# Performance work log

Measured on AMD Instinct MI355X. Metric: run time of the kernel, lower is better.

## Reference

```python
import jax, jax.numpy as jnp
import numpy as np

N = 4096          # num_nodes
M = 131072        # num_edges (chain + random)
H = 64            # hidden_size of DerivConstrainedPerceptron
DMIN = 0.5
DMAX = 2.0
LO = 1.0 / DMAX   # min slope of h_inv
HI = 1.0 / DMIN   # max slope of h_inv
MITR = 30         # fixed iteration count (early-exit at eps in the original; 30 iters converge far below eps here)
RIDGE = 1e-6      # numerical ridge on grounded Laplacian


def _h_inv(y, logits, w_raw, b):
    # Derivative-constrained perceptron: h_inv'(y) = LO + (HI-LO)*sum_k p_k*sigmoid(w_k*y+b_k) in (LO, HI).
    p = jax.nn.softmax(logits)                     # (H,)
    w = jax.nn.softplus(w_raw) + 1e-3              # (H,) positive slopes
    s = jax.nn.softplus(y[..., None] * w + b)      # (m, d, H)
    return LO * y + (HI - LO) * jnp.einsum('mdh,h->md', s, p / w)


def _chol_grounded(src, dst, w, n):
    # Dense weighted graph Laplacian L = A diag(w) A^T built by scatter-add, grounded at the last node.
    L = jnp.zeros((n, n), w.dtype)
    L = L.at[src, src].add(w).at[dst, dst].add(w)
    L = L.at[src, dst].add(-w).at[dst, src].add(-w)
    Lg = L[:-1, :-1] + RIDGE * jnp.eye(n - 1, dtype=w.dtype)
    return jnp.linalg.cholesky(Lg)


def _solve_grounded(c, rhs):
    # Solve L phi = rhs with the grounded node's potential fixed to 0 (valid for balanced rhs; only
    # potential differences phi[src]-phi[dst] are used, which equal A^T L^+ rhs).
    x = jax.scipy.linalg.cho_solve((c, True), rhs[:-1])
    return jnp.concatenate([x, jnp.zeros((1, rhs.shape[1]), rhs.dtype)], axis=0)


def _forward(u, edge_weights, logits, w_raw, b, src, dst):
    n = u.shape[0]
    w = edge_weights
    wcol = w[:, None]
    U = u[:, None]                                  # (n, 1) balanced injections
    At = lambda phi: phi[src] - phi[dst]            # incidence^T: node potentials -> edge diffs
    Amap = lambda z: jnp.zeros((n, z.shape[1]), z.dtype).at[src].add(z).at[dst].add(-z)  # incidence
    # get_f_cut: min-norm flow with A f_cut = U (unweighted Laplacian pseudo-solve)
    c0 = _chol_grounded(src, dst, jnp.ones_like(w), n)
    f_cut = At(_solve_grounded(c0, U))
    # weighted Laplacian factor for cycle_projection
    cw = _chol_grounded(src, dst, w, n)

    def cycle_projection(z):
        phi = _solve_grounded(cw, Amap(z))
        return z - wcol * At(phi)

    def step(f_cyc, _):
        y = (f_cyc + f_cut) / wcol
        z = f_cyc - DMIN * wcol * _h_inv(y, logits, w_raw, b)
        return cycle_projection(z), None

    f_cyc, _ = jax.lax.scan(step, jnp.zeros_like(f_cut), None, length=MITR)
    return (f_cyc + f_cut)[:, 0]                    # (m,) flows, squeezed as in IFNLayer.forward


def setup_inputs() -> dict:
    key = jax.random.key(0)
    k1, k2, k3, k4, k5, k6, k7 = jax.random.split(key, 7)
    # connected graph: chain spanning tree + random extra edges (no self-loops)
    src0 = jnp.arange(N - 1, dtype=jnp.int32)
    dst0 = src0 + 1
    extra = M - (N - 1)
    src1 = jax.random.randint(k1, (extra,), 0, N, dtype=jnp.int32)
    off = jax.random.randint(k2, (extra,), 1, N, dtype=jnp.int32)
    dst1 = (src1 + off) % N
    src = jnp.concatenate([src0, src1])
    dst = jnp.concatenate([dst0, dst1])
    edge_weights = 0.5 + jax.random.uniform(k3, (M,), jnp.float32)
    u = jax.random.normal(k4, (N,), jnp.float32)
    u = u - u.mean()                                # balanced nodal injections
    logits = 0.1 * jax.random.normal(k5, (H,), jnp.float32)
    w_raw = 0.1 * jax.random.normal(k6, (H,), jnp.float32)
    b = 0.1 * jax.random.normal(k7, (H,), jnp.float32)
    return {"u": u, "edge_weights": edge_weights, "logits": logits,
            "w_raw": w_raw, "b": b, "src": src, "dst": dst}


def reference(u, edge_weights, logits, w_raw, b, src, dst):
    return _forward(u, edge_weights, logits, w_raw, b, src, dst)
```

## Files before the change

kernel.cpp:

```cpp
#include <hip/hip_runtime.h>

#define NN 4096
#define MM 131072
#define HH 64
#define NB 128
#define NT 1024
#define NTH (NB*NT)
#define FB 512
#define FT 256
#define LPN 32
#define ELP 4
#define SLOTC 112
#define MITR 13
#define NPOL 1
#define CURS 16
#define TBL 4096
#define YMIN (-64.0f)
#define YMAX (64.0f)
#define INV_DY 32.0f

#define THETA 1.025f

static_assert(NTH == LPN*NN, "lanes-per-node mapping requires NTH == LPN*N");
static_assert(MM == FB*FT,   "one edge per thread in fill kernel");
static_assert(NN % NT == 0,  "LDS snapshot staging loop requires NN % NT == 0");
static_assert(HH == 32*2,    "htab build uses 32 lanes x 2 heads");
static_assert(ELP*LPN >= SLOTC, "register CSR must cover slot capacity");

constexpr size_t OFF_FLAGS = 0;
constexpr size_t OFF_CUR   = 1024;
constexpr size_t ZERO_BYTES = OFF_CUR + (size_t)NN*CURS*4;
constexpr size_t OFF_HTAB  = ZERO_BYTES;
constexpr size_t OFF_P0    = OFF_HTAB + 4104*4;
constexpr size_t OFF_P1    = OFF_P0   + NN*8;
constexpr size_t OFF_P2    = OFF_P1   + NN*8;
constexpr size_t OFF_SLOT  = OFF_P2   + NN*8;

__device__ __forceinline__ int cload_i(const int* p) {
    return __hip_atomic_load(p, __ATOMIC_RELAXED, __HIP_MEMORY_SCOPE_AGENT);
}
__device__ __forceinline__ unsigned long long cload64(const unsigned long long* p) {
    return __hip_atomic_load(p, __ATOMIC_RELAXED, __HIP_MEMORY_SCOPE_AGENT);
}
__device__ __forceinline__ void cstore64(unsigned long long* p, unsigned long long v) {
    __hip_atomic_store(p, v, __ATOMIC_RELAXED, __HIP_MEMORY_SCOPE_AGENT);
}
__device__ __forceinline__ unsigned long long pack2(float a, float b) {
    return ((unsigned long long)__float_as_uint(b) << 32) | __float_as_uint(a);
}

__device__ __forceinline__ float hinv_lds(float y, const float* __restrict__ hs) {
    float v;
    if (y <= YMIN) {
        v = hs[0];
    } else if (y >= YMAX) {
        v = hs[TBL] + (y - YMAX) * 1.5f;
    } else {
        float t = (y - YMIN) * INV_DY;
        int i = (int)t;
        if (i > TBL-1) i = TBL-1;
        float fr = t - (float)i;
        float h0 = hs[i];
        v = h0 + (hs[i+1] - h0) * fr;
    }
    return 0.5f*y + v;
}

__device__ __forceinline__ void fast_sync() {
    asm volatile("s_waitcnt lgkmcnt(0)" ::: "memory");
    __builtin_amdgcn_s_barrier();
    __builtin_amdgcn_sched_barrier(0);
}

__device__ __forceinline__ void exec_sync() {
    __builtin_amdgcn_sched_barrier(0);
    __builtin_amdgcn_s_barrier();
    __builtin_amdgcn_sched_barrier(0);
}

__device__ __forceinline__ void grid_bar_full(int* flags, int& phase) {
    __syncthreads();
    phase += 1;
    if (threadIdx.x == 0) {
        __hip_atomic_store(&flags[blockIdx.x], phase,
                           __ATOMIC_RELAXED, __HIP_MEMORY_SCOPE_AGENT);
    }
    if (threadIdx.x < 64) {
        int lane = threadIdx.x;
        for (;;) {
            int a = cload_i(&flags[lane]);
            int b = cload_i(&flags[lane+64]);
            if (min(a, b) >= phase) break;
            __builtin_amdgcn_s_sleep(1);
        }
    }
    __syncthreads();
}

__global__ __launch_bounds__(FT) void fill_kernel(
    const float* __restrict__ ew,
    const int* __restrict__ src, const int* __restrict__ dst,
    const float* __restrict__ logits, const float* __restrict__ w_raw,
    const float* __restrict__ bb,
    char* __restrict__ ws)
{
    int*   cur   = (int*)  (ws + OFF_CUR);
    float* htab  = (float*)(ws + OFF_HTAB);
    unsigned long long* slots = (unsigned long long*)(ws + OFF_SLOT);

    const int g = blockIdx.x*FT + threadIdx.x;

    int a0 = src[g], d0 = dst[g];
    float w0 = ew[g];
    int p0 = atomicAdd(&cur[a0*CURS], 1);
    int p1 = atomicAdd(&cur[d0*CURS], 1);
    unsigned long long wb0 = ((unsigned long long)__float_as_uint(w0)) << 32;
    slots[(size_t)a0*SLOTC + p0] = wb0 | (unsigned int)(d0 | (g << 12));
    slots[(size_t)d0*SLOTC + p1] =
        wb0 | ((unsigned int)(a0 | (g << 12)) | 0x80000000u);

    {
        const int e0 = g >> 5;
        const int hl = (g & 31) << 1;
        float ex0 = expf(logits[hl+0]);
        float ex1 = expf(logits[hl+1]);
        float dsum = ex0 + ex1;
        dsum += __shfl_xor(dsum, 1);  dsum += __shfl_xor(dsum, 2);
        dsum += __shfl_xor(dsum, 4);  dsum += __shfl_xor(dsum, 8);
        dsum += __shfl_xor(dsum, 16);
        float wh0 = log1pf(expf(w_raw[hl+0])) + 0.001f;
        float wh1 = log1pf(expf(w_raw[hl+1])) + 0.001f;
        float c0 = (ex0/dsum)/wh0, c1 = (ex1/dsum)/wh1;
        float b0 = bb[hl+0], b1 = bb[hl+1];

        auto entry_acc = [&](float y) {
            float x0 = y*wh0 + b0, x1 = y*wh1 + b1;
            float sp0 = (x0 > 20.f) ? x0 : log1pf(expf(x0));
            float sp1 = (x1 > 20.f) ? x1 : log1pf(expf(x1));
            return c0*sp0 + c1*sp1;
        };

        float acc = entry_acc(YMIN + (float)e0 * (1.0f/INV_DY));
        acc += __shfl_xor(acc, 1);  acc += __shfl_xor(acc, 2);
        acc += __shfl_xor(acc, 4);  acc += __shfl_xor(acc, 8);
        acc += __shfl_xor(acc, 16);
        if ((g & 31) == 0) htab[e0] = 1.5f * acc;
        if (e0 == 0) {
            float acc2 = entry_acc(YMAX);
            acc2 += __shfl_xor(acc2, 1);  acc2 += __shfl_xor(acc2, 2);
            acc2 += __shfl_xor(acc2, 4);  acc2 += __shfl_xor(acc2, 8);
            acc2 += __shfl_xor(acc2, 16);
            if ((g & 31) == 0) htab[TBL] = 1.5f * acc2;
        }
    }
}

__global__ __launch_bounds__(NT) void main_kernel(
    const float* __restrict__ u,
    char* __restrict__ ws, float* __restrict__ out)
{
    int*   flags = (int*)  (ws + OFF_FLAGS);
    const int*   cur  = (const int*)  (ws + OFF_CUR);
    const float* htab = (const float*)(ws + OFF_HTAB);
    unsigned long long* P[3] = {
        (unsigned long long*)(ws + OFF_P0),
        (unsigned long long*)(ws + OFF_P1),
        (unsigned long long*)(ws + OFF_P2) };
    const unsigned long long* slots = (const unsigned long long*)(ws + OFF_SLOT);

    const int tid = threadIdx.x;
    const int g   = blockIdx.x*NT + tid;
    const int n   = g / LPN;
    const int s   = g % LPN;
    int phase = 0;

    __shared__ float hs[TBL+1];
    __shared__ unsigned long long ps[NN];

    for (int t = tid; t <= TBL; t += NT) hs[t] = htab[t];

    float u_reg = (s == 0) ? u[n] : 0.f;

    unsigned long long vraw[ELP];
    #pragma unroll
    for (int j = 0; j < ELP; ++j) {
        int sl = s + j*LPN;
        int slc = (sl < SLOTC) ? sl : (SLOTC-1);
        vraw[j] = slots[(size_t)n*SLOTC + slc];
    }
    const int   deg = cur[n*CURS];
    const float dg0 = (float)deg;

    int   cidx[ELP];
    float cw[ELP];
    float cwinv[ELP];
    float cmask[ELP];
    float csgn[ELP];
    int   ceid[ELP];
    float zz_s[ELP];
    #pragma unroll
    for (int j = 0; j < ELP; ++j) {
        int sl  = s + j*LPN;
        bool ok = sl < deg;
        unsigned long long v = ok ? vraw[j] : 0ull;
        unsigned int meta = (unsigned int)v;
        float w  = ok ? __uint_as_float((unsigned int)(v >> 32)) : 0.f;
        int   c  = (int)(meta & 0xFFFu);
        cidx[j]  = c;
        cw[j]    = w;
        ceid[j]  = (int)((meta >> 12) & 0x1FFFFu);
        csgn[j]  = ok ? (((int)meta < 0) ? -1.f : 1.f) : 0.f;
        cmask[j] = ok ? 1.f : 0.f;
        cwinv[j] = ok ? 1.0f / w : 0.f;
        zz_s[j]  = 0.f;
    }
    float wdn = 0.f;
    #pragma unroll
    for (int j = 0; j < ELP; ++j) wdn += cw[j];
    wdn += __shfl_xor(wdn, 1);  wdn += __shfl_xor(wdn, 2);
    wdn += __shfl_xor(wdn, 4);  wdn += __shfl_xor(wdn, 8);
    wdn += __shfl_xor(wdn, 16);

    float phiw_reg = 0.f;
    float phi0_reg = 0.f;
    const float inv_tw = 1.0f / (THETA * wdn);
    const float inv_t0 = 1.0f / (THETA * dg0);

    __syncthreads();

    int cb = 0;
    unsigned long long pf[NN/NT];

    for (int it = 0; it < MITR + NPOL; ++it) {
        const bool zact = (it < MITR);

        if (it > 0) {
            #pragma unroll
            for (int k = 0; k < NN/NT; ++k) ps[tid + k*NT] = pf[k];
        }
        float phiw_self = __shfl(phiw_reg, 0, LPN);
        float phi0_self = __shfl(phi0_reg, 0, LPN);
        if (it > 0) fast_sync();

        float acc0 = 0.f;
        float accr = 0.f;
        #pragma unroll
        for (int j = 0; j < ELP; ++j) {
            unsigned long long v = (it > 0) ? ps[cidx[j]] : 0ull;
            float pw = __uint_as_float((unsigned int)v);
            float p0 = __uint_as_float((unsigned int)(v >> 32));
            acc0 += cmask[j] * p0;
            float dphi = csgn[j] * (phiw_self - pw);
            float z;
            if (zact) {
                float fcut = csgn[j] * (phi0_self - p0);
                float fc = (it == 0) ? 0.f : (zz_s[j] - cw[j]*dphi);
                float y = (fc + fcut) * cwinv[j];
                float h = hinv_lds(y, hs);
                z = fc - 0.5f*cw[j]*h;
                zz_s[j] = z;
            } else {
                z = zz_s[j];
            }
            accr += csgn[j] * (z - cw[j]*dphi);
        }
        acc0 += __shfl_xor(acc0, 1);  acc0 += __shfl_xor(acc0, 2);
        acc0 += __shfl_xor(acc0, 4);  acc0 += __shfl_xor(acc0, 8);
        acc0 += __shfl_xor(acc0, 16);
        accr += __shfl_xor(accr, 1);  accr += __shfl_xor(accr, 2);
        accr += __shfl_xor(accr, 4);  accr += __shfl_xor(accr, 8);
        accr += __shfl_xor(accr, 16);
        if (s == 0) {
            float r0 = u_reg - (dg0*phi0_reg - acc0);
            phi0_reg += r0 * inv_t0;
            phiw_reg += accr * inv_tw;
            cstore64(&P[(cb+1)%3][n], pack2(phiw_reg, phi0_reg));
        }

        if (it == 0) {
            grid_bar_full(flags, phase);
            #pragma unroll
            for (int k = 0; k < NN/NT; ++k)
                pf[k] = cload64(&P[(cb+1)%3][tid + k*NT]);
        } else if (it < MITR + NPOL - 1) {
            exec_sync();
            phase += 1;
            if (tid == 0) {
                __hip_atomic_store(&flags[blockIdx.x], phase,
                                   __ATOMIC_RELAXED, __HIP_MEMORY_SCOPE_AGENT);
            }
            __builtin_amdgcn_sched_barrier(0);
            #pragma unroll
            for (int k = 0; k < NN/NT; ++k)
                pf[k] = cload64(&P[(cb+1)%3][tid + k*NT]);
            if (tid < 64) {
                int need = phase - ((it == MITR - 1) ? 1 : 2);
                for (;;) {
                    int a = cload_i(&flags[tid]);
                    int b = cload_i(&flags[tid+64]);
                    if (min(a, b) >= need) break;
                    __builtin_amdgcn_s_sleep(1);
                }
            }
        } else {
            grid_bar_full(flags, phase);
        }
        cb = (cb + 1) % 3;
    }

    {
        #pragma unroll
        for (int k = 0; k < NN/NT; ++k) {
            int t = tid + k*NT;
            ps[t] = cload64(&P[cb][t]);
        }
        float phiw_self = __shfl(phiw_reg, 0, LPN);
        float phi0_self = __shfl(phi0_reg, 0, LPN);
        __syncthreads();
        #pragma unroll
        for (int j = 0; j < ELP; ++j) {
            if (csgn[j] > 0.5f) {
                unsigned long long v = ps[cidx[j]];
                float pw = __uint_as_float((unsigned int)v);
                float p0 = __uint_as_float((unsigned int)(v >> 32));
                float dphi = phiw_self - pw;
                float fcut = phi0_self - p0;
                float fc   = zz_s[j] - cw[j]*dphi;
                out[ceid[j]] = fc + fcut;
            }
        }
    }
}

extern "C" void kernel_launch(void* const* d_in, const int* in_sizes, int n_in,
                              void* d_out, int out_size, void* d_ws, size_t ws_size,
                              hipStream_t stream) {
    const float* u      = (const float*)d_in[0];
    const float* ew     = (const float*)d_in[1];
    const float* logits = (const float*)d_in[2];
    const float* w_raw  = (const float*)d_in[3];
    const float* b      = (const float*)d_in[4];
    const int*   src    = (const int*)d_in[5];
    const int*   dst    = (const int*)d_in[6];
    float* out = (float*)d_out;
    char* ws = (char*)d_ws;

    hipMemsetAsync(ws, 0, ZERO_BYTES, stream);
    fill_kernel<<<FB, FT, 0, stream>>>(ew, src, dst, logits, w_raw, b, ws);
    main_kernel<<<NB, NT, 0, stream>>>(u, ws, out);
}
```

Baseline: 148.8 us.

## Build CSR slots via split-counter count, prefix and scatter passes

Replaces the single fill kernel, which used one atomic cursor per node, with three passes. A count pass spreads atomics over 16 sub-counters per node (keyed by edge index), a prefix pass turns those counts into per-node bases, and a scatter pass writes each slot from its base plus rank. The aim is to cut atomic contention on hot node cursors. In exchange it adds two kernel launches, an extra memset and extra global traffic for the rank array. The main kernel's first-iteration full grid barrier is also replaced by the relaxed barrier path, relying on a zeroed P1 buffer.

```diff
diff --git a/kernel.cpp b/kernel.cpp
--- a/kernel.cpp
+++ b/kernel.cpp
@@ -6,14 +6,14 @@
 #define NB 128
 #define NT 1024
 #define NTH (NB*NT)
-#define FB 512
-#define FT 256
 #define LPN 32
 #define ELP 4
 #define SLOTC 112
 #define MITR 13
 #define NPOL 1
-#define CURS 16
+#define SPLIT 16
+#define FB 1024
+#define FT 256
 #define TBL 4096
 #define YMIN (-64.0f)
 #define YMAX (64.0f)
@@ -22,19 +22,24 @@
 #define THETA 1.025f
 
 static_assert(NTH == LPN*NN, "lanes-per-node mapping requires NTH == LPN*N");
-static_assert(MM == FB*FT,   "one edge per thread in fill kernel");
+static_assert(2*MM == FB*FT, "one edge-side per thread in fill kernels");
 static_assert(NN % NT == 0,  "LDS snapshot staging loop requires NN % NT == 0");
 static_assert(HH == 32*2,    "htab build uses 32 lanes x 2 heads");
 static_assert(ELP*LPN >= SLOTC, "register CSR must cover slot capacity");
+static_assert((MM % SPLIT) == 0, "q = e & (SPLIT-1) identical for both sides");
 
 constexpr size_t OFF_FLAGS = 0;
-constexpr size_t OFF_CUR   = 1024;
-constexpr size_t ZERO_BYTES = OFF_CUR + (size_t)NN*CURS*4;
-constexpr size_t OFF_HTAB  = ZERO_BYTES;
+constexpr size_t OFF_CNT   = 1024;
+constexpr size_t ZERO_BYTES = OFF_CNT + (size_t)NN*SPLIT*4;
+constexpr size_t OFF_CUR   = ZERO_BYTES;
+constexpr size_t OFF_BASE  = OFF_CUR  + NN*4;
+constexpr size_t OFF_RANK  = OFF_BASE + (size_t)NN*SPLIT*4;
+constexpr size_t OFF_HTAB  = OFF_RANK + (size_t)2*MM*4;
 constexpr size_t OFF_P0    = OFF_HTAB + 4104*4;
 constexpr size_t OFF_P1    = OFF_P0   + NN*8;
 constexpr size_t OFF_P2    = OFF_P1   + NN*8;
 constexpr size_t OFF_SLOT  = OFF_P2   + NN*8;
+static_assert(OFF_P0 % 8 == 0 && OFF_SLOT % 8 == 0, "u64 alignment");
 
 __device__ __forceinline__ int cload_i(const int* p) {
     return __hip_atomic_load(p, __ATOMIC_RELAXED, __HIP_MEMORY_SCOPE_AGENT);
@@ -72,12 +77,6 @@
     __builtin_amdgcn_sched_barrier(0);
 }
 
-__device__ __forceinline__ void exec_sync() {
-    __builtin_amdgcn_sched_barrier(0);
-    __builtin_amdgcn_s_barrier();
-    __builtin_amdgcn_sched_barrier(0);
-}
-
 __device__ __forceinline__ void grid_bar_full(int* flags, int& phase) {
     __syncthreads();
     phase += 1;
@@ -97,29 +96,24 @@
     __syncthreads();
 }
 
-__global__ __launch_bounds__(FT) void fill_kernel(
-    const float* __restrict__ ew,
+__global__ __launch_bounds__(FT) void count_kernel(
     const int* __restrict__ src, const int* __restrict__ dst,
     const float* __restrict__ logits, const float* __restrict__ w_raw,
     const float* __restrict__ bb,
     char* __restrict__ ws)
 {
-    int*   cur   = (int*)  (ws + OFF_CUR);
-    float* htab  = (float*)(ws + OFF_HTAB);
-    unsigned long long* slots = (unsigned long long*)(ws + OFF_SLOT);
-
-    const int g = blockIdx.x*FT + threadIdx.x;
-
-    int a0 = src[g], d0 = dst[g];
-    float w0 = ew[g];
-    int p0 = atomicAdd(&cur[a0*CURS], 1);
-    int p1 = atomicAdd(&cur[d0*CURS], 1);
-    unsigned long long wb0 = ((unsigned long long)__float_as_uint(w0)) << 32;
-    slots[(size_t)a0*SLOTC + p0] = wb0 | (unsigned int)(d0 | (g << 12));
-    slots[(size_t)d0*SLOTC + p1] =
-        wb0 | ((unsigned int)(a0 | (g << 12)) | 0x80000000u);
-
-    {
+    int* cnt    = (int*)(ws + OFF_CNT);
+    int* rankA  = (int*)(ws + OFF_RANK);
+    float* htab = (float*)(ws + OFF_HTAB);
+
+    const int g    = blockIdx.x*FT + threadIdx.x;
+    const int e    = g & (MM-1);
+    const int side = g >> 17;
+    const int node = side ? dst[e] : src[e];
+    const int q    = e & (SPLIT-1);
+    rankA[g] = atomicAdd(&cnt[node*SPLIT + q], 1);
+
+    if (g < TBL*32) {
         const int e0 = g >> 5;
         const int hl = (g & 31) << 1;
         float ex0 = expf(logits[hl+0]);
@@ -155,6 +149,44 @@
     }
 }
 
+__global__ __launch_bounds__(1024) void prefix_kernel(char* __restrict__ ws)
+{
+    const int n = blockIdx.x*1024 + threadIdx.x;
+    if (n >= NN) return;
+    const int* cnt = (const int*)(ws + OFF_CNT);
+    int* base = (int*)(ws + OFF_BASE);
+    int* cur  = (int*)(ws + OFF_CUR);
+    int run = 0;
+    #pragma unroll
+    for (int q = 0; q < SPLIT; ++q) {
+        base[n*SPLIT + q] = run;
+        run += cnt[n*SPLIT + q];
+    }
+    cur[n] = run;
+}
+
+__global__ __launch_bounds__(FT) void scatter_kernel(
+    const float* __restrict__ ew,
+    const int* __restrict__ src, const int* __restrict__ dst,
+    char* __restrict__ ws)
+{
+    const int* base = (const int*)(ws + OFF_BASE);
+    const int* rankA = (const int*)(ws + OFF_RANK);
+    unsigned long long* slots = (unsigned long long*)(ws + OFF_SLOT);
+
+    const int g    = blockIdx.x*FT + threadIdx.x;
+    const int e    = g & (MM-1);
+    const int side = g >> 17;
+    const int a = src[e], d = dst[e];
+    const int node = side ? d : a;
+    const int q    = e & (SPLIT-1);
+    const int sl   = base[node*SPLIT + q] + rankA[g];
+    unsigned long long wb = ((unsigned long long)__float_as_uint(ew[e])) << 32;
+    unsigned int meta = side ? ((unsigned int)(a | (e << 12)) | 0x80000000u)
+                             : (unsigned int)(d | (e << 12));
+    slots[(size_t)node*SLOTC + sl] = wb | meta;
+}
+
 __global__ __launch_bounds__(NT) void main_kernel(
     const float* __restrict__ u,
     char* __restrict__ ws, float* __restrict__ out)
@@ -188,7 +220,7 @@
         int slc = (sl < SLOTC) ? sl : (SLOTC-1);
         vraw[j] = slots[(size_t)n*SLOTC + slc];
     }
-    const int   deg = cur[n*CURS];
+    const int   deg = cur[n];
     const float dg0 = (float)deg;
 
     int   cidx[ELP];
@@ -276,14 +308,8 @@
             phiw_reg += accr * inv_tw;
             cstore64(&P[(cb+1)%3][n], pack2(phiw_reg, phi0_reg));
         }
-
-        if (it == 0) {
-            grid_bar_full(flags, phase);
-            #pragma unroll
-            for (int k = 0; k < NN/NT; ++k)
-                pf[k] = cload64(&P[(cb+1)%3][tid + k*NT]);
-        } else if (it < MITR + NPOL - 1) {
-            exec_sync();
+        if (it < MITR + NPOL - 1) {
+            __syncthreads();
             phase += 1;
             if (tid == 0) {
                 __hip_atomic_store(&flags[blockIdx.x], phase,
@@ -346,6 +372,9 @@
     char* ws = (char*)d_ws;
 
     hipMemsetAsync(ws, 0, ZERO_BYTES, stream);
-    fill_kernel<<<FB, FT, 0, stream>>>(ew, src, dst, logits, w_raw, b, ws);
+    hipMemsetAsync(ws + OFF_P1, 0, NN*8, stream);
+    count_kernel<<<FB, FT, 0, stream>>>(src, dst, logits, w_raw, b, ws);
+    prefix_kernel<<<(NN+1023)/1024, 1024, 0, stream>>>(ws);
+    scatter_kernel<<<FB, FT, 0, stream>>>(ew, src, dst, ws);
     main_kernel<<<NB, NT, 0, stream>>>(u, ws, out);
 }
```

After: 160.0 us. 7.5% more time.
